# Performance work log

Hardware: AMD Instinct MI355X
Metric: run time of the kernel (lower is better)

The kernel has to match this reference:

```python
import jax, jax.numpy as jnp
import numpy as np

B, P, N, E = 4, 4, 4096, 512
QKV_DIM, HEADS = 512, 8
DH = QKV_DIM // HEADS
EPS = 1e-12  # F.normalize default eps


def setup_inputs() -> dict:
    key = jax.random.key(0)
    ks = jax.random.split(key, 5)
    s = 1.0 / np.sqrt(E)
    return {
        "x": jax.random.normal(ks[0], (B, P, N, E), dtype=jnp.float32),
        "w_qkv": jax.random.normal(ks[1], (3 * QKV_DIM, E), dtype=jnp.float32) * s,
        "b_qkv": jax.random.normal(ks[2], (3 * QKV_DIM,), dtype=jnp.float32) * 0.01,
        "temperature": jnp.ones((HEADS, 1, 1), dtype=jnp.float32),
        "w_out": jax.random.normal(ks[3], (E, QKV_DIM), dtype=jnp.float32) * (1.0 / np.sqrt(QKV_DIM)),
        "b_out": jax.random.normal(ks[4], (E,), dtype=jnp.float32) * 0.01,
    }


def _l2norm(t):
    # F.normalize(t, dim=-1): t / max(||t||_2, eps)
    n = jnp.sqrt(jnp.sum(t * t, axis=-1, keepdims=True))
    return t / jnp.maximum(n, EPS)


def reference(x, w_qkv, b_qkv, temperature, w_out, b_out):
    b, p, n, _ = x.shape
    qkv = x @ w_qkv.T + b_qkv                      # (b,p,n,3*qkv)
    q, k, v = jnp.split(qkv, 3, axis=-1)
    def to_heads(t):
        # (b,p,n,h*dh) -> (b,p,h,dh,n)  (channels-as-tokens)
        t = t.reshape(b, p, n, HEADS, DH)
        return jnp.transpose(t, (0, 1, 3, 4, 2))
    q, k, v = to_heads(q), to_heads(k), to_heads(v)
    q = _l2norm(q)                                  # normalize over tokens n
    k = _l2norm(k)
    # channel-wise (dh x dh) attention per head, temperature-scaled
    attn = jnp.einsum('bphdn,bphen->bphde', q, k) * temperature  # (b,p,h,dh,dh)
    attn = jax.nn.softmax(attn, axis=-1)
    out = jnp.einsum('bphde,bphen->bphdn', attn, v)               # (b,p,h,dh,n)
    # torch rearrange 'b p h n d -> b p d (h n)' on (b,p,h,dh,n) -> (b,p,n,h*dh)
    out = jnp.transpose(out, (0, 1, 4, 2, 3)).reshape(b, p, n, HEADS * DH)
    return out @ w_out.T + b_out
```

## Files before the change

### kernel.cpp

```cpp
#include <hip/hip_runtime.h>
#include <stdint.h>

typedef unsigned short u16;
typedef __bf16 bf16x8 __attribute__((ext_vector_type(8)));
typedef float f32x4 __attribute__((ext_vector_type(4)));

#define AS1 __attribute__((address_space(1)))
#define AS3 __attribute__((address_space(3)))

__device__ __forceinline__ void gload_lds16(u16* lds_wave_base, const u16* g) {
  __builtin_amdgcn_global_load_lds((AS1 void*)g, (AS3 void*)lds_wave_base, 16, 0, 0);
}

__device__ __forceinline__ u16 f2bf(float f) {
  unsigned int u = __float_as_uint(f);
  u += 0x7fffu + ((u >> 16) & 1u);
  return (u16)(u >> 16);
}

__global__ void cast_f32_bf16(const float* __restrict__ in, u16* __restrict__ out, int n8) {
  int i = blockIdx.x * blockDim.x + threadIdx.x;
  if (i >= n8) return;
  const float4* p = (const float4*)in + (size_t)i * 2;
  float4 a = p[0], b = p[1];
  uint2 lo, hi;
  lo.x = (unsigned)f2bf(a.x) | ((unsigned)f2bf(a.y) << 16);
  lo.y = (unsigned)f2bf(a.z) | ((unsigned)f2bf(a.w) << 16);
  hi.x = (unsigned)f2bf(b.x) | ((unsigned)f2bf(b.y) << 16);
  hi.y = (unsigned)f2bf(b.z) | ((unsigned)f2bf(b.w) << 16);
  uint2* o = (uint2*)out + (size_t)i * 2;
  o[0] = lo;
  o[1] = hi;
}

template <int MODE>
__global__ __launch_bounds__(256) void gemm_bt(const u16* __restrict__ gA,
                                               const u16* __restrict__ gB,
                                               const float* __restrict__ bias,
                                               void* __restrict__ gC,
                                               float* __restrict__ ssq) {
  __shared__ __align__(16) u16 smem[128 * 136];
  u16* As = smem;
  u16* Bs = smem + 4096;
  const int t = threadIdx.x;
  const int w = t >> 6, l = t & 63;
  const int lrow = l & 15, quad = l >> 4;
  const int wm = (w >> 1) * 64, wn = (w & 1) * 64;
  int m0, n0, zz = 0;
  if (MODE == 0) {
    const int b = blockIdx.x;
    const int ch = (b >> 3) & 7;
    const int T = ((b >> 6) << 3) | (b & 7);
    m0 = T * 128;
    n0 = ch * 128;
  } else if (MODE == 1) {
    const int b = blockIdx.x;
    const int j = (b >> 3) & 3;
    const int T = ((b >> 5) << 3) | (b & 7);
    m0 = j * 128;
    n0 = T * 128;
  } else {
    const int b = blockIdx.x;
    const int local = b & 127;
    zz = b >> 7;
    const int j = (local >> 3) & 3;
    const int T = ((local >> 5) << 3) | (local & 7);
    m0 = j * 128;
    n0 = T * 128;
  }
  const u16* pA = gA;
  const u16* pB = gB;
  if (MODE == 2) {
    pA += (size_t)zz * (512 * 512);
    pB += (size_t)zz * (4096 * 512);
  }
  const int srow = w * 32 + (l >> 2);
  const int scol = (l & 3) * 8;
  const u16* ga0 = pA + (size_t)(m0 + srow) * 512 + scol;
  const u16* ga1 = pA + (size_t)(m0 + srow + 16) * 512 + scol;
  const u16* gb0 = pB + (size_t)(n0 + srow) * 512 + scol;
  const u16* gb1 = pB + (size_t)(n0 + srow + 16) * 512 + scol;
  u16* lA0 = &As[w * 1024];
  u16* lA1 = &As[w * 1024 + 512];
  u16* lB0 = &Bs[w * 1024];
  u16* lB1 = &Bs[w * 1024 + 512];

  f32x4 acc[4][4];
#pragma unroll
  for (int mi = 0; mi < 4; ++mi)
#pragma unroll
    for (int ni = 0; ni < 4; ++ni) acc[mi][ni] = (f32x4){0.f, 0.f, 0.f, 0.f};

#pragma unroll 1
  for (int k0 = 0; k0 < 512; k0 += 32) {
    gload_lds16(lA0, ga0 + k0);
    gload_lds16(lA1, ga1 + k0);
    gload_lds16(lB0, gb0 + k0);
    gload_lds16(lB1, gb1 + k0);
    __syncthreads();
    bf16x8 af[4], bfr[4];
#pragma unroll
    for (int mi = 0; mi < 4; ++mi)
      af[mi] = *(const bf16x8*)&As[(wm + mi * 16 + lrow) * 32 + quad * 8];
#pragma unroll
    for (int ni = 0; ni < 4; ++ni)
      bfr[ni] = *(const bf16x8*)&Bs[(wn + ni * 16 + lrow) * 32 + quad * 8];
#pragma unroll
    for (int mi = 0; mi < 4; ++mi)
#pragma unroll
      for (int ni = 0; ni < 4; ++ni)
        acc[mi][ni] = __builtin_amdgcn_mfma_f32_16x16x32_bf16(af[mi], bfr[ni], acc[mi][ni], 0, 0, 0);
    __syncthreads();
  }

  if (MODE == 2) {
    float* fs = (float*)smem;
#pragma unroll
    for (int half = 0; half < 2; ++half) {
      if (half) __syncthreads();
#pragma unroll
      for (int mi = 0; mi < 4; ++mi) {
        const int mrow_l = wm + mi * 16 + quad * 4;
        const float4 bb = *(const float4*)&bias[m0 + mrow_l];
#pragma unroll
        for (int ni = 0; ni < 4; ++ni) {
          const int ncol_l = wn + ni * 16 + lrow;
          if ((ncol_l >> 6) != half) continue;
          f32x4 v = acc[mi][ni];
          float4 o;
          o.x = v[0] + bb.x;
          o.y = v[1] + bb.y;
          o.z = v[2] + bb.z;
          o.w = v[3] + bb.w;
          *(float4*)&fs[(ncol_l & 63) * 136 + mrow_l] = o;
        }
      }
      __syncthreads();
#pragma unroll
      for (int j2 = 0; j2 < 4; ++j2) {
        const int g = j2 * 256 + t;
        const int r = g >> 4;
        const int c = (g & 15) * 8;
        float4 v0 = *(const float4*)&fs[r * 136 + c];
        float4 v1 = *(const float4*)&fs[r * 136 + c + 4];
        float* yp = (float*)gC + (((size_t)zz * 4096 + n0 + half * 64 + r) * 512 + m0 + c);
        *(float4*)yp = v0;
        *(float4*)(yp + 4) = v1;
      }
    }
  } else {
    float ss[4] = {0.f, 0.f, 0.f, 0.f};
#pragma unroll
    for (int mi = 0; mi < 4; ++mi) {
      const int mrow_l = wm + mi * 16 + quad * 4;
#pragma unroll
      for (int ni = 0; ni < 4; ++ni) {
        const int ncol_l = wn + ni * 16 + lrow;
        f32x4 v = acc[mi][ni];
        float f0, f1, f2, f3;
        if (MODE == 0) {
          const float bb = bias[n0 + ncol_l];
          f0 = v[0] + bb;
          f1 = v[1] + bb;
          f2 = v[2] + bb;
          f3 = v[3] + bb;
          ss[ni] += f0 * f0 + f1 * f1 + f2 * f2 + f3 * f3;
        } else {
          const float4 bb = *(const float4*)&bias[1024 + m0 + mrow_l];
          f0 = v[0] + bb.x;
          f1 = v[1] + bb.y;
          f2 = v[2] + bb.z;
          f3 = v[3] + bb.w;
        }
        uint2 pk;
        pk.x = (unsigned)f2bf(f0) | ((unsigned)f2bf(f1) << 16);
        pk.y = (unsigned)f2bf(f2) | ((unsigned)f2bf(f3) << 16);
        *(uint2*)&smem[ncol_l * 136 + mrow_l] = pk;
      }
    }
    if (MODE == 0) {
#pragma unroll
      for (int ni = 0; ni < 4; ++ni) {
        float s = ss[ni];
        s += __shfl_xor(s, 16);
        s += __shfl_xor(s, 32);
        if (quad == 0)
          atomicAdd(&ssq[((m0 >> 12) << 10) + n0 + wn + ni * 16 + lrow], s);
      }
    }
    __syncthreads();
    u16* outp = (u16*)gC;
#pragma unroll
    for (int j = 0; j < 8; ++j) {
      const int g = j * 256 + t;
      const int r = g >> 4;
      const int c = (g & 15) * 8;
      uint4 val = *(const uint4*)&smem[r * 136 + c];
      size_t gaddr;
      if (MODE == 0) {
        gaddr = ((size_t)(m0 >> 12) << 22) + ((size_t)(n0 + r) << 12) + (size_t)((m0 & 4095) + c);
      } else {
        const int tokg = n0 + r;
        gaddr = (size_t)(tokg >> 12) * (4096 * 512) + (size_t)(tokg & 4095) * 512 + (size_t)(m0 + c);
      }
      *(uint4*)(outp + gaddr) = val;
    }
  }
}

__global__ __launch_bounds__(256) void qk_partial(const u16* __restrict__ QKt,
                                                  float* __restrict__ part) {
  __shared__ __align__(16) float sred[64 * 64];
  const int b = blockIdx.x;
  const int chunk = b & 7, blk = b >> 3;
  const int bp = blk >> 3, h = blk & 7;
  const int t = threadIdx.x, w = t >> 6, l = t & 63;
  const int lrow = l & 15, quad = l >> 4;
  const u16* base = QKt + ((size_t)bp << 22);
  const u16* qb = base + ((size_t)(h * 64) << 12);
  const u16* kb = base + ((size_t)(512 + h * 64) << 12);
  f32x4 acc[4][4];
#pragma unroll
  for (int mi = 0; mi < 4; ++mi)
#pragma unroll
    for (int ni = 0; ni < 4; ++ni) acc[mi][ni] = (f32x4){0.f, 0.f, 0.f, 0.f};
  const int nbase = chunk * 512 + w * 128;
#pragma unroll 1
  for (int ks = 0; ks < 4; ++ks) {
    const int nn = nbase + ks * 32 + quad * 8;
    bf16x8 af[4], bfr[4];
#pragma unroll
    for (int mi = 0; mi < 4; ++mi)
      af[mi] = *(const bf16x8*)(qb + (((size_t)(mi * 16 + lrow)) << 12) + nn);
#pragma unroll
    for (int ni = 0; ni < 4; ++ni)
      bfr[ni] = *(const bf16x8*)(kb + (((size_t)(ni * 16 + lrow)) << 12) + nn);
#pragma unroll
    for (int mi = 0; mi < 4; ++mi)
#pragma unroll
      for (int ni = 0; ni < 4; ++ni)
        acc[mi][ni] = __builtin_amdgcn_mfma_f32_16x16x32_bf16(af[mi], bfr[ni], acc[mi][ni], 0, 0, 0);
  }
  __syncthreads();
  for (int ww = 0; ww < 4; ++ww) {
    if (w == ww) {
#pragma unroll
      for (int mi = 0; mi < 4; ++mi)
#pragma unroll
        for (int ni = 0; ni < 4; ++ni)
#pragma unroll
          for (int r = 0; r < 4; ++r) {
            const int idx = (mi * 16 + quad * 4 + r) * 64 + ni * 16 + lrow;
            if (ww == 0)
              sred[idx] = acc[mi][ni][r];
            else
              sred[idx] += acc[mi][ni][r];
          }
    }
    __syncthreads();
  }
  float4* dst = (float4*)(part + ((size_t)blk * 8 + chunk) * 4096);
  const float4* src = (const float4*)sred;
  for (int i = t; i < 1024; i += 256) dst[i] = src[i];
}

__global__ __launch_bounds__(512) void softmax_weff(const float* __restrict__ part,
                                                    const u16* __restrict__ wout,
                                                    const float* __restrict__ temperature,
                                                    const float* __restrict__ ssq,
                                                    u16* __restrict__ Weff) {
  __shared__ __align__(16) float sattn[64 * 64];
  __shared__ __align__(16) u16 sattnT[64 * 64];
  __shared__ float rn[128];
  const int blk = blockIdx.x;
  const int bp = blk >> 3, h = blk & 7;
  const int t = threadIdx.x, w = t >> 6, l = t & 63;
  const int lrow = l & 15, quad = l >> 4;

  const float4* pbase = (const float4*)(part + (size_t)blk * 8 * 4096);
  for (int i = t; i < 1024; i += 512) {
    float4 s0 = pbase[i];
#pragma unroll
    for (int p = 1; p < 8; ++p) {
      float4 sp = pbase[p * 1024 + i];
      s0.x += sp.x;
      s0.y += sp.y;
      s0.z += sp.z;
      s0.w += sp.w;
    }
    ((float4*)sattn)[i] = s0;
  }

  if (t < 128) {
    const int ch = (t < 64) ? (h * 64 + t) : (448 + h * 64 + t);
    const float nn = sqrtf(ssq[(bp << 10) + ch]);
    rn[t] = 1.f / fmaxf(nn, 1e-12f);
  }
  __syncthreads();

  if (t < 64) {
    const int d = t;
    const float rq = rn[d];
    const float tmp = temperature[h];
    float mx = -1e30f;
    for (int e = 0; e < 64; ++e) {
      const int idx = (e + d) & 63;
      float v = sattn[d * 64 + idx] * rq * rn[64 + idx] * tmp;
      sattn[d * 64 + idx] = v;
      mx = fmaxf(mx, v);
    }
    float s = 0.f;
    for (int e = 0; e < 64; ++e) {
      const int idx = (e + d) & 63;
      float p = __expf(sattn[d * 64 + idx] - mx);
      s += p;
      sattn[d * 64 + idx] = p;
    }
    const float inv = 1.f / s;
    for (int e = 0; e < 64; ++e) sattnT[e * 64 + d] = f2bf(sattn[d * 64 + e] * inv);
  }
  __syncthreads();

  bf16x8 a0[4], a1[4];
#pragma unroll
  for (int mi = 0; mi < 4; ++mi) {
    a0[mi] = *(const bf16x8*)&sattnT[(mi * 16 + lrow) * 64 + quad * 8];
    a1[mi] = *(const bf16x8*)&sattnT[(mi * 16 + lrow) * 64 + 32 + quad * 8];
  }
  u16* wb = Weff + ((size_t)bp * (512 * 512));
#pragma unroll 1
  for (int nb = 0; nb < 4; ++nb) {
    const int co = (w * 4 + nb) * 16 + lrow;
    const u16* wrow = wout + (size_t)co * 512 + h * 64;
    bf16x8 b0 = *(const bf16x8*)(wrow + quad * 8);
    bf16x8 b1 = *(const bf16x8*)(wrow + 32 + quad * 8);
#pragma unroll
    for (int mi = 0; mi < 4; ++mi) {
      f32x4 c = (f32x4){0.f, 0.f, 0.f, 0.f};
      c = __builtin_amdgcn_mfma_f32_16x16x32_bf16(a0[mi], b0, c, 0, 0, 0);
      c = __builtin_amdgcn_mfma_f32_16x16x32_bf16(a1[mi], b1, c, 0, 0, 0);
      const int e0 = mi * 16 + quad * 4;
      uint2 pk;
      pk.x = (unsigned)f2bf(c[0]) | ((unsigned)f2bf(c[1]) << 16);
      pk.y = (unsigned)f2bf(c[2]) | ((unsigned)f2bf(c[3]) << 16);
      *(uint2*)(wb + (size_t)co * 512 + h * 64 + e0) = pk;
    }
  }
}

extern "C" void kernel_launch(void* const* d_in, const int* in_sizes, int n_in,
                              void* d_out, int out_size, void* d_ws, size_t ws_size,
                              hipStream_t stream) {
  const float* x      = (const float*)d_in[0];
  const float* w_qkv  = (const float*)d_in[1];
  const float* b_qkv  = (const float*)d_in[2];
  const float* temp   = (const float*)d_in[3];
  const float* w_out  = (const float*)d_in[4];
  const float* b_out  = (const float*)d_in[5];
  float* y = (float*)d_out;

  char* ws = (char*)d_ws;
  u16* x_bf    = (u16*)(ws);
  u16* wqkv_bf = (u16*)(ws + 67108864);
  u16* wout_bf = (u16*)(ws + 68681728);
  u16* QKt     = (u16*)(ws + 69206016);
  u16* V_nat   = (u16*)(ws + 203423744);
  u16* Weff    = (u16*)(ws + 270532608);
  float* ssq   = (float*)(ws + 278921216);
  float* part  = (float*)(ws);

  hipMemsetAsync(ssq, 0, 16 * 1024 * sizeof(float), stream);
  cast_f32_bf16<<<16384, 256, 0, stream>>>(x, x_bf, 33554432 / 8);
  cast_f32_bf16<<<384, 256, 0, stream>>>(w_qkv, wqkv_bf, 786432 / 8);
  cast_f32_bf16<<<128, 256, 0, stream>>>(w_out, wout_bf, 262144 / 8);

  gemm_bt<0><<<4096, 256, 0, stream>>>(x_bf, wqkv_bf, b_qkv, QKt, ssq);
  gemm_bt<1><<<2048, 256, 0, stream>>>(wqkv_bf + 1024 * 512, x_bf, b_qkv, V_nat, nullptr);
  qk_partial<<<1024, 256, 0, stream>>>(QKt, part);
  softmax_weff<<<128, 512, 0, stream>>>(part, wout_bf, temp, ssq, Weff);
  gemm_bt<2><<<2048, 256, 0, stream>>>(Weff, V_nat, b_out, y, nullptr);
}
```

Before: 509.7 us.

## Reassociate attention via input Gram matrix and fold projections into a fused weight

The QKV projection over all tokens is replaced by the per-(b,p) Gram matrix S = X^T X (512x512, split-K with a reduction kernel). Q·K^T is then derived as Wq S Wk^T plus bias correction terms, and the token L2 norms come from diag(W S W^T) plus column sums of x. The V projection is folded into a combined weight M = Weff·Wv, so the final pass is a single GEMM of x with M plus a precomputed bias vector. This removes the large Q/K/V intermediates and their GEMMs at the cost of a transposed copy of x, a 4096-deep Gram GEMM, a hi/lo bf16 split of S to limit precision loss, and several extra small kernels.

```diff
diff --git a/kernel.cpp b/kernel.cpp
--- a/kernel.cpp
+++ b/kernel.cpp
@@ -16,6 +16,11 @@
   unsigned int u = __float_as_uint(f);
   u += 0x7fffu + ((u >> 16) & 1u);
   return (u16)(u >> 16);
+}
+__device__ __forceinline__ float bf2f(u16 h) { return __uint_as_float(((unsigned)h) << 16); }
+
+__device__ __forceinline__ int swz(int e, int n) {
+  return e * 136 + (((n >> 3) ^ (e & 15)) << 3) + (n & 7);
 }
 
 __global__ void cast_f32_bf16(const float* __restrict__ in, u16* __restrict__ out, int n8) {
@@ -33,12 +38,91 @@
   o[1] = hi;
 }
 
+__global__ __launch_bounds__(256) void cast_x_dual(const float* __restrict__ x,
+                                                   u16* __restrict__ xbf,
+                                                   u16* __restrict__ xbfT,
+                                                   float* __restrict__ svec) {
+  __shared__ __align__(16) u16 sm[128 * 136];
+  const int b = blockIdx.x;
+  const int bp = b >> 7;
+  const int tt = (b >> 2) & 31;
+  const int et = b & 3;
+  const int t = threadIdx.x;
+  const int n0 = tt * 128, e0 = et * 128;
+  const int rsub = t >> 5;
+  const int c4 = (t & 31) * 4;
+  float cs0 = 0.f, cs1 = 0.f, cs2 = 0.f, cs3 = 0.f;
+  const float* xb = x + ((size_t)bp * 4096 + n0) * 512 + e0;
+  u16* ob = xbf + ((size_t)bp * 4096 + n0) * 512 + e0;
+#pragma unroll
+  for (int j = 0; j < 16; ++j) {
+    const int r = j * 8 + rsub;
+    float4 v = *(const float4*)(xb + (size_t)r * 512 + c4);
+    u16 b0 = f2bf(v.x), b1 = f2bf(v.y), b2 = f2bf(v.z), b3 = f2bf(v.w);
+    uint2 pk;
+    pk.x = (unsigned)b0 | ((unsigned)b1 << 16);
+    pk.y = (unsigned)b2 | ((unsigned)b3 << 16);
+    *(uint2*)(ob + (size_t)r * 512 + c4) = pk;
+    sm[(c4 + 0) * 136 + ((j ^ ((c4 + 0) & 15)) << 3) + rsub] = b0;
+    sm[(c4 + 1) * 136 + ((j ^ ((c4 + 1) & 15)) << 3) + rsub] = b1;
+    sm[(c4 + 2) * 136 + ((j ^ ((c4 + 2) & 15)) << 3) + rsub] = b2;
+    sm[(c4 + 3) * 136 + ((j ^ ((c4 + 3) & 15)) << 3) + rsub] = b3;
+    cs0 += v.x; cs1 += v.y; cs2 += v.z; cs3 += v.w;
+  }
+  cs0 += __shfl_xor(cs0, 32);
+  cs1 += __shfl_xor(cs1, 32);
+  cs2 += __shfl_xor(cs2, 32);
+  cs3 += __shfl_xor(cs3, 32);
+  if ((t & 63) < 32) {
+    float* sp = svec + (size_t)bp * 512 + e0 + c4;
+    atomicAdd(sp + 0, cs0);
+    atomicAdd(sp + 1, cs1);
+    atomicAdd(sp + 2, cs2);
+    atomicAdd(sp + 3, cs3);
+  }
+  __syncthreads();
+  u16* otb = xbfT + ((size_t)bp * 512 + e0) * 4096 + n0;
+#pragma unroll
+  for (int j = 0; j < 8; ++j) {
+    const int re = j * 16 + (t >> 4);
+    const int ct8 = t & 15;
+    uint4 v = *(const uint4*)&sm[re * 136 + ((ct8 ^ (re & 15)) << 3)];
+    *(uint4*)(otb + (size_t)re * 4096 + ct8 * 8) = v;
+  }
+}
+
+__global__ __launch_bounds__(256) void transpose_wv(const float* __restrict__ wv,
+                                                    u16* __restrict__ wvT) {
+  __shared__ __align__(16) u16 sm[128 * 136];
+  const int b = blockIdx.x;
+  const int r0 = (b >> 2) * 128;
+  const int c0 = (b & 3) * 128;
+  const int t = threadIdx.x;
+  const int rsub = t >> 5, c4 = (t & 31) * 4;
+#pragma unroll
+  for (int j = 0; j < 16; ++j) {
+    const int r = j * 8 + rsub;
+    float4 v = *(const float4*)(wv + (size_t)(r0 + r) * 512 + c0 + c4);
+    sm[(c4 + 0) * 136 + ((j ^ ((c4 + 0) & 15)) << 3) + rsub] = f2bf(v.x);
+    sm[(c4 + 1) * 136 + ((j ^ ((c4 + 1) & 15)) << 3) + rsub] = f2bf(v.y);
+    sm[(c4 + 2) * 136 + ((j ^ ((c4 + 2) & 15)) << 3) + rsub] = f2bf(v.z);
+    sm[(c4 + 3) * 136 + ((j ^ ((c4 + 3) & 15)) << 3) + rsub] = f2bf(v.w);
+  }
+  __syncthreads();
+#pragma unroll
+  for (int j = 0; j < 8; ++j) {
+    const int re = j * 16 + (t >> 4);
+    const int ct8 = t & 15;
+    uint4 v = *(const uint4*)&sm[re * 136 + ((ct8 ^ (re & 15)) << 3)];
+    *(uint4*)(wvT + (size_t)(c0 + re) * 512 + r0 + ct8 * 8) = v;
+  }
+}
+
 template <int MODE>
-__global__ __launch_bounds__(256) void gemm_bt(const u16* __restrict__ gA,
-                                               const u16* __restrict__ gB,
-                                               const float* __restrict__ bias,
-                                               void* __restrict__ gC,
-                                               float* __restrict__ ssq) {
+__global__ __launch_bounds__(256) void gemm5(const u16* __restrict__ gA,
+                                             const u16* __restrict__ gB,
+                                             const float* __restrict__ bias,
+                                             void* __restrict__ gC) {
   __shared__ __align__(16) u16 smem[128 * 136];
   u16* As = smem;
   u16* Bs = smem + 4096;
@@ -46,44 +130,61 @@
   const int w = t >> 6, l = t & 63;
   const int lrow = l & 15, quad = l >> 4;
   const int wm = (w >> 1) * 64, wn = (w & 1) * 64;
-  int m0, n0, zz = 0;
+  int m0, n0, bp = 0, kc = 0;
   if (MODE == 0) {
     const int b = blockIdx.x;
-    const int ch = (b >> 3) & 7;
-    const int T = ((b >> 6) << 3) | (b & 7);
-    m0 = T * 128;
-    n0 = ch * 128;
+    bp = b >> 6;
+    kc = b & 3;
+    const int tl = (b >> 2) & 15;
+    m0 = (tl >> 2) * 128;
+    n0 = (tl & 3) * 128;
   } else if (MODE == 1) {
     const int b = blockIdx.x;
-    const int j = (b >> 3) & 3;
-    const int T = ((b >> 5) << 3) | (b & 7);
-    m0 = j * 128;
-    n0 = T * 128;
+    bp = b >> 5;
+    const int tl = b & 31;
+    m0 = (tl >> 2) * 128;
+    n0 = (tl & 3) * 128;
+  } else if (MODE == 2) {
+    const int b = blockIdx.x;
+    bp = b >> 4;
+    const int tl = b & 15;
+    m0 = (tl >> 2) * 128;
+    n0 = (tl & 3) * 128;
   } else {
     const int b = blockIdx.x;
     const int local = b & 127;
-    zz = b >> 7;
+    bp = b >> 7;
     const int j = (local >> 3) & 3;
     const int T = ((local >> 5) << 3) | (local & 7);
     m0 = j * 128;
     n0 = T * 128;
   }
+  constexpr int LDA = (MODE == 0) ? 4096 : 512;
+  constexpr int LDB = (MODE == 0) ? 4096 : 512;
   const u16* pA = gA;
   const u16* pB = gB;
-  if (MODE == 2) {
-    pA += (size_t)zz * (512 * 512);
-    pB += (size_t)zz * (4096 * 512);
+  if (MODE == 0) {
+    pA += (size_t)bp * (512 * 4096);
+    pB = pA;
+  } else if (MODE == 1) {
+    pB += (size_t)bp * (512 * 512);
+  } else if (MODE == 2) {
+    pA += (size_t)bp * (512 * 512);
+  } else {
+    pA += (size_t)bp * (512 * 512);
+    pB += (size_t)bp * (4096 * 512);
   }
   const int srow = w * 32 + (l >> 2);
   const int scol = (l & 3) * 8;
-  const u16* ga0 = pA + (size_t)(m0 + srow) * 512 + scol;
-  const u16* ga1 = pA + (size_t)(m0 + srow + 16) * 512 + scol;
-  const u16* gb0 = pB + (size_t)(n0 + srow) * 512 + scol;
-  const u16* gb1 = pB + (size_t)(n0 + srow + 16) * 512 + scol;
+  const int koff = (MODE == 0) ? kc * 1024 : 0;
+  const u16* ga0 = pA + (size_t)(m0 + srow) * LDA + scol + koff;
+  const u16* ga1 = ga0 + (size_t)16 * LDA;
+  const u16* gb0 = pB + (size_t)(n0 + srow) * LDB + scol + koff;
+  const u16* gb1 = gb0 + (size_t)16 * LDB;
   u16* lA0 = &As[w * 1024];
-  u16* lA1 = &As[w * 1024 + 512];
+  u16* lA1 = lA0 + 512;
   u16* lB0 = &Bs[w * 1024];
-  u16* lB1 = &Bs[w * 1024 + 512];
+  u16* lB1 = lB0 + 512;
 
   f32x4 acc[4][4];
 #pragma unroll
@@ -91,29 +192,40 @@
 #pragma unroll
     for (int ni = 0; ni < 4; ++ni) acc[mi][ni] = (f32x4){0.f, 0.f, 0.f, 0.f};
 
+  constexpr int KLEN = (MODE == 0) ? 1024 : 512;
+  constexpr int NPH = (MODE == 1) ? 2 : 1;
 #pragma unroll 1
-  for (int k0 = 0; k0 < 512; k0 += 32) {
-    gload_lds16(lA0, ga0 + k0);
-    gload_lds16(lA1, ga1 + k0);
-    gload_lds16(lB0, gb0 + k0);
-    gload_lds16(lB1, gb1 + k0);
-    __syncthreads();
-    bf16x8 af[4], bfr[4];
-#pragma unroll
-    for (int mi = 0; mi < 4; ++mi)
-      af[mi] = *(const bf16x8*)&As[(wm + mi * 16 + lrow) * 32 + quad * 8];
-#pragma unroll
-    for (int ni = 0; ni < 4; ++ni)
-      bfr[ni] = *(const bf16x8*)&Bs[(wn + ni * 16 + lrow) * 32 + quad * 8];
-#pragma unroll
-    for (int mi = 0; mi < 4; ++mi)
+  for (int ph = 0; ph < NPH; ++ph) {
+    const size_t boff = (MODE == 1) ? (size_t)ph * 4194304 : 0;
+#pragma unroll 1
+    for (int k0 = 0; k0 < KLEN; k0 += 32) {
+      gload_lds16(lA0, ga0 + k0);
+      gload_lds16(lA1, ga1 + k0);
+      gload_lds16(lB0, gb0 + boff + k0);
+      gload_lds16(lB1, gb1 + boff + k0);
+      __syncthreads();
+      bf16x8 af[4], bfr[4];
+#pragma unroll
+      for (int mi = 0; mi < 4; ++mi)
+        af[mi] = *(const bf16x8*)&As[(wm + mi * 16 + lrow) * 32 + quad * 8];
 #pragma unroll
       for (int ni = 0; ni < 4; ++ni)
-        acc[mi][ni] = __builtin_amdgcn_mfma_f32_16x16x32_bf16(af[mi], bfr[ni], acc[mi][ni], 0, 0, 0);
-    __syncthreads();
-  }
-
-  if (MODE == 2) {
+        bfr[ni] = *(const bf16x8*)&Bs[(wn + ni * 16 + lrow) * 32 + quad * 8];
+#pragma unroll
+      for (int mi = 0; mi < 4; ++mi)
+#pragma unroll
+        for (int ni = 0; ni < 4; ++ni)
+          acc[mi][ni] = __builtin_amdgcn_mfma_f32_16x16x32_bf16(af[mi], bfr[ni], acc[mi][ni], 0, 0, 0);
+      __syncthreads();
+    }
+  }
+
+  if (MODE == 0 || MODE == 3) {
+    float* gCp;
+    if (MODE == 0)
+      gCp = (float*)gC + (size_t)(kc * 16 + bp) * 262144;
+    else
+      gCp = (float*)gC + (size_t)bp * (4096 * 512);
     float* fs = (float*)smem;
 #pragma unroll
     for (int half = 0; half < 2; ++half) {
@@ -121,7 +233,8 @@
 #pragma unroll
       for (int mi = 0; mi < 4; ++mi) {
         const int mrow_l = wm + mi * 16 + quad * 4;
-        const float4 bb = *(const float4*)&bias[m0 + mrow_l];
+        float4 bb = {0.f, 0.f, 0.f, 0.f};
+        if (MODE == 3) bb = *(const float4*)&bias[(size_t)bp * 512 + m0 + mrow_l];
 #pragma unroll
         for (int ni = 0; ni < 4; ++ni) {
           const int ncol_l = wn + ni * 16 + lrow;
@@ -143,13 +256,13 @@
         const int c = (g & 15) * 8;
         float4 v0 = *(const float4*)&fs[r * 136 + c];
         float4 v1 = *(const float4*)&fs[r * 136 + c + 4];
-        float* yp = (float*)gC + (((size_t)zz * 4096 + n0 + half * 64 + r) * 512 + m0 + c);
+        float* yp = gCp + ((size_t)(n0 + half * 64 + r) * 512 + m0 + c);
         *(float4*)yp = v0;
         *(float4*)(yp + 4) = v1;
       }
     }
   } else {
-    float ss[4] = {0.f, 0.f, 0.f, 0.f};
+    u16* gCp = (u16*)gC + ((MODE == 1) ? (size_t)bp * 524288 : (size_t)bp * 262144);
 #pragma unroll
     for (int mi = 0; mi < 4; ++mi) {
       const int mrow_l = wm + mi * 16 + quad * 4;
@@ -157,155 +270,143 @@
       for (int ni = 0; ni < 4; ++ni) {
         const int ncol_l = wn + ni * 16 + lrow;
         f32x4 v = acc[mi][ni];
-        float f0, f1, f2, f3;
-        if (MODE == 0) {
-          const float bb = bias[n0 + ncol_l];
-          f0 = v[0] + bb;
-          f1 = v[1] + bb;
-          f2 = v[2] + bb;
-          f3 = v[3] + bb;
-          ss[ni] += f0 * f0 + f1 * f1 + f2 * f2 + f3 * f3;
-        } else {
-          const float4 bb = *(const float4*)&bias[1024 + m0 + mrow_l];
-          f0 = v[0] + bb.x;
-          f1 = v[1] + bb.y;
-          f2 = v[2] + bb.z;
-          f3 = v[3] + bb.w;
-        }
-        uint2 pk;
-        pk.x = (unsigned)f2bf(f0) | ((unsigned)f2bf(f1) << 16);
-        pk.y = (unsigned)f2bf(f2) | ((unsigned)f2bf(f3) << 16);
-        *(uint2*)&smem[ncol_l * 136 + mrow_l] = pk;
+        smem[(mrow_l + 0) * 136 + ncol_l] = f2bf(v[0]);
+        smem[(mrow_l + 1) * 136 + ncol_l] = f2bf(v[1]);
+        smem[(mrow_l + 2) * 136 + ncol_l] = f2bf(v[2]);
+        smem[(mrow_l + 3) * 136 + ncol_l] = f2bf(v[3]);
       }
     }
-    if (MODE == 0) {
-#pragma unroll
-      for (int ni = 0; ni < 4; ++ni) {
-        float s = ss[ni];
-        s += __shfl_xor(s, 16);
-        s += __shfl_xor(s, 32);
-        if (quad == 0)
-          atomicAdd(&ssq[((m0 >> 12) << 10) + n0 + wn + ni * 16 + lrow], s);
-      }
-    }
     __syncthreads();
-    u16* outp = (u16*)gC;
 #pragma unroll
     for (int j = 0; j < 8; ++j) {
       const int g = j * 256 + t;
       const int r = g >> 4;
       const int c = (g & 15) * 8;
       uint4 val = *(const uint4*)&smem[r * 136 + c];
-      size_t gaddr;
-      if (MODE == 0) {
-        gaddr = ((size_t)(m0 >> 12) << 22) + ((size_t)(n0 + r) << 12) + (size_t)((m0 & 4095) + c);
-      } else {
-        const int tokg = n0 + r;
-        gaddr = (size_t)(tokg >> 12) * (4096 * 512) + (size_t)(tokg & 4095) * 512 + (size_t)(m0 + c);
-      }
-      *(uint4*)(outp + gaddr) = val;
-    }
-  }
-}
-
-__global__ __launch_bounds__(256) void qk_partial(const u16* __restrict__ QKt,
-                                                  float* __restrict__ part) {
-  __shared__ __align__(16) float sred[64 * 64];
-  const int b = blockIdx.x;
-  const int chunk = b & 7, blk = b >> 3;
-  const int bp = blk >> 3, h = blk & 7;
-  const int t = threadIdx.x, w = t >> 6, l = t & 63;
-  const int lrow = l & 15, quad = l >> 4;
-  const u16* base = QKt + ((size_t)bp << 22);
-  const u16* qb = base + ((size_t)(h * 64) << 12);
-  const u16* kb = base + ((size_t)(512 + h * 64) << 12);
-  f32x4 acc[4][4];
-#pragma unroll
-  for (int mi = 0; mi < 4; ++mi)
-#pragma unroll
-    for (int ni = 0; ni < 4; ++ni) acc[mi][ni] = (f32x4){0.f, 0.f, 0.f, 0.f};
-  const int nbase = chunk * 512 + w * 128;
-#pragma unroll 1
-  for (int ks = 0; ks < 4; ++ks) {
-    const int nn = nbase + ks * 32 + quad * 8;
-    bf16x8 af[4], bfr[4];
-#pragma unroll
-    for (int mi = 0; mi < 4; ++mi)
-      af[mi] = *(const bf16x8*)(qb + (((size_t)(mi * 16 + lrow)) << 12) + nn);
-#pragma unroll
-    for (int ni = 0; ni < 4; ++ni)
-      bfr[ni] = *(const bf16x8*)(kb + (((size_t)(ni * 16 + lrow)) << 12) + nn);
-#pragma unroll
-    for (int mi = 0; mi < 4; ++mi)
-#pragma unroll
-      for (int ni = 0; ni < 4; ++ni)
-        acc[mi][ni] = __builtin_amdgcn_mfma_f32_16x16x32_bf16(af[mi], bfr[ni], acc[mi][ni], 0, 0, 0);
-  }
-  __syncthreads();
-  for (int ww = 0; ww < 4; ++ww) {
-    if (w == ww) {
-#pragma unroll
-      for (int mi = 0; mi < 4; ++mi)
-#pragma unroll
-        for (int ni = 0; ni < 4; ++ni)
-#pragma unroll
-          for (int r = 0; r < 4; ++r) {
-            const int idx = (mi * 16 + quad * 4 + r) * 64 + ni * 16 + lrow;
-            if (ww == 0)
-              sred[idx] = acc[mi][ni][r];
-            else
-              sred[idx] += acc[mi][ni][r];
-          }
-    }
-    __syncthreads();
-  }
-  float4* dst = (float4*)(part + ((size_t)blk * 8 + chunk) * 4096);
-  const float4* src = (const float4*)sred;
-  for (int i = t; i < 1024; i += 256) dst[i] = src[i];
-}
-
-__global__ __launch_bounds__(512) void softmax_weff(const float* __restrict__ part,
-                                                    const u16* __restrict__ wout,
-                                                    const float* __restrict__ temperature,
-                                                    const float* __restrict__ ssq,
-                                                    u16* __restrict__ Weff) {
+      *(uint4*)(gCp + (size_t)(m0 + r) * 512 + n0 + c) = val;
+    }
+  }
+}
+
+__global__ __launch_bounds__(256) void s4red(const float* __restrict__ Spart,
+                                             u16* __restrict__ Shi) {
+  const size_t i = ((size_t)blockIdx.x * 256 + threadIdx.x) * 4;
+  if (i >= 4194304) return;
+  float4 a = *(const float4*)(Spart + i);
+  float4 b = *(const float4*)(Spart + 4194304 + i);
+  float4 c = *(const float4*)(Spart + 2 * 4194304 + i);
+  float4 d = *(const float4*)(Spart + 3 * 4194304 + i);
+  float s0 = a.x + b.x + c.x + d.x;
+  float s1 = a.y + b.y + c.y + d.y;
+  float s2 = a.z + b.z + c.z + d.z;
+  float s3 = a.w + b.w + c.w + d.w;
+  u16 h0 = f2bf(s0), h1 = f2bf(s1), h2 = f2bf(s2), h3 = f2bf(s3);
+  uint2 hp;
+  hp.x = (unsigned)h0 | ((unsigned)h1 << 16);
+  hp.y = (unsigned)h2 | ((unsigned)h3 << 16);
+  *(uint2*)(Shi + i) = hp;
+  uint2 lp;
+  lp.x = (unsigned)f2bf(s0 - bf2f(h0)) | ((unsigned)f2bf(s1 - bf2f(h1)) << 16);
+  lp.y = (unsigned)f2bf(s2 - bf2f(h2)) | ((unsigned)f2bf(s3 - bf2f(h3)) << 16);
+  *(uint2*)(Shi + 4194304 + i) = lp;
+}
+
+__device__ __forceinline__ void bf8_expand(uint4 v, float* o) {
+  o[0] = bf2f((u16)(v.x & 0xffff)); o[1] = bf2f((u16)(v.x >> 16));
+  o[2] = bf2f((u16)(v.y & 0xffff)); o[3] = bf2f((u16)(v.y >> 16));
+  o[4] = bf2f((u16)(v.z & 0xffff)); o[5] = bf2f((u16)(v.z >> 16));
+  o[6] = bf2f((u16)(v.w & 0xffff)); o[7] = bf2f((u16)(v.w >> 16));
+}
+
+__global__ __launch_bounds__(512) void softmax_weff2(const u16* __restrict__ P,
+                                                     const u16* __restrict__ wqkv,
+                                                     const float* __restrict__ b_qkv,
+                                                     const float* __restrict__ svec,
+                                                     const float* __restrict__ temperature,
+                                                     const u16* __restrict__ wout,
+                                                     u16* __restrict__ Weff) {
   __shared__ __align__(16) float sattn[64 * 64];
   __shared__ __align__(16) u16 sattnT[64 * 64];
-  __shared__ float rn[128];
+  __shared__ float ub[128], dq[128], rnA[128], bb[128];
   const int blk = blockIdx.x;
   const int bp = blk >> 3, h = blk & 7;
   const int t = threadIdx.x, w = t >> 6, l = t & 63;
   const int lrow = l & 15, quad = l >> 4;
 
-  const float4* pbase = (const float4*)(part + (size_t)blk * 8 * 4096);
-  for (int i = t; i < 1024; i += 512) {
-    float4 s0 = pbase[i];
-#pragma unroll
-    for (int p = 1; p < 8; ++p) {
-      float4 sp = pbase[p * 1024 + i];
-      s0.x += sp.x;
-      s0.y += sp.y;
-      s0.z += sp.z;
-      s0.w += sp.w;
-    }
-    ((float4*)sattn)[i] = s0;
-  }
+  {
+    const int mi = w >> 1;
+    const int nip = (w & 1) * 2;
+    const u16* arow = P + ((size_t)bp * 1024 + h * 64 + mi * 16 + lrow) * 512;
+    const u16* brow0 = wqkv + ((size_t)(512 + h * 64 + nip * 16 + lrow)) * 512;
+    const u16* brow1 = brow0 + 16 * 512;
+    f32x4 c0 = (f32x4){0.f, 0.f, 0.f, 0.f};
+    f32x4 c1 = (f32x4){0.f, 0.f, 0.f, 0.f};
+#pragma unroll 1
+    for (int ks = 0; ks < 16; ++ks) {
+      const int ko = ks * 32 + quad * 8;
+      bf16x8 a = *(const bf16x8*)(arow + ko);
+      bf16x8 b0 = *(const bf16x8*)(brow0 + ko);
+      bf16x8 b1 = *(const bf16x8*)(brow1 + ko);
+      c0 = __builtin_amdgcn_mfma_f32_16x16x32_bf16(a, b0, c0, 0, 0, 0);
+      c1 = __builtin_amdgcn_mfma_f32_16x16x32_bf16(a, b1, c1, 0, 0, 0);
+    }
+    const int drow = mi * 16 + quad * 4;
+#pragma unroll
+    for (int r = 0; r < 4; ++r) {
+      sattn[(drow + r) * 64 + nip * 16 + lrow] = c0[r];
+      sattn[(drow + r) * 64 + (nip + 1) * 16 + lrow] = c1[r];
+    }
+  }
+
+  {
+    const int rr = t >> 2, sub = t & 3;
+    const int c = (rr < 64) ? (h * 64 + rr) : (512 + h * 64 + (rr - 64));
+    const u16* prow = P + ((size_t)bp * 1024 + c) * 512 + sub * 128;
+    const u16* wrow = wqkv + (size_t)c * 512 + sub * 128;
+    const float* sv = svec + (size_t)bp * 512 + sub * 128;
+    float accp = 0.f, accu = 0.f;
+#pragma unroll 1
+    for (int i = 0; i < 128; i += 8) {
+      float pf[8], wf[8];
+      bf8_expand(*(const uint4*)(prow + i), pf);
+      bf8_expand(*(const uint4*)(wrow + i), wf);
+      float4 s0 = *(const float4*)(sv + i);
+      float4 s1 = *(const float4*)(sv + i + 4);
+      accp += pf[0] * wf[0] + pf[1] * wf[1] + pf[2] * wf[2] + pf[3] * wf[3] +
+              pf[4] * wf[4] + pf[5] * wf[5] + pf[6] * wf[6] + pf[7] * wf[7];
+      accu += wf[0] * s0.x + wf[1] * s0.y + wf[2] * s0.z + wf[3] * s0.w +
+              wf[4] * s1.x + wf[5] * s1.y + wf[6] * s1.z + wf[7] * s1.w;
+    }
+    accp += __shfl_xor(accp, 1);
+    accp += __shfl_xor(accp, 2);
+    accu += __shfl_xor(accu, 1);
+    accu += __shfl_xor(accu, 2);
+    if (sub == 0) {
+      dq[rr] = accp;
+      ub[rr] = accu;
+    }
+  }
+  __syncthreads();
 
   if (t < 128) {
-    const int ch = (t < 64) ? (h * 64 + t) : (448 + h * 64 + t);
-    const float nn = sqrtf(ssq[(bp << 10) + ch]);
-    rn[t] = 1.f / fmaxf(nn, 1e-12f);
+    const int c = (t < 64) ? (h * 64 + t) : (512 + h * 64 + (t - 64));
+    const float bc = b_qkv[c];
+    const float ss = dq[t] + 2.f * bc * ub[t] + 4096.f * bc * bc;
+    rnA[t] = 1.f / fmaxf(sqrtf(ss), 1e-12f);
+    bb[t] = bc;
   }
   __syncthreads();
 
   if (t < 64) {
     const int d = t;
-    const float rq = rn[d];
+    const float rq = rnA[d], uqv = ub[d], bq = bb[d];
     const float tmp = temperature[h];
     float mx = -1e30f;
     for (int e = 0; e < 64; ++e) {
       const int idx = (e + d) & 63;
-      float v = sattn[d * 64 + idx] * rq * rn[64 + idx] * tmp;
+      const float bk = bb[64 + idx];
+      float g = sattn[d * 64 + idx] + bq * ub[64 + idx] + bk * uqv + 4096.f * bq * bk;
+      float v = g * rq * rnA[64 + idx] * tmp;
       sattn[d * 64 + idx] = v;
       mx = fmaxf(mx, v);
     }
@@ -317,7 +418,10 @@
       sattn[d * 64 + idx] = p;
     }
     const float inv = 1.f / s;
-    for (int e = 0; e < 64; ++e) sattnT[e * 64 + d] = f2bf(sattn[d * 64 + e] * inv);
+    for (int e = 0; e < 64; ++e) {
+      const int idx = (e + d) & 63;
+      sattnT[idx * 64 + d] = f2bf(sattn[d * 64 + idx] * inv);
+    }
   }
   __syncthreads();
 
@@ -348,35 +452,60 @@
   }
 }
 
+__global__ __launch_bounds__(512) void yb_kernel(const u16* __restrict__ Weff,
+                                                 const float* __restrict__ b_qkv,
+                                                 const float* __restrict__ b_out,
+                                                 float* __restrict__ yb) {
+  const int bp = blockIdx.x, co = threadIdx.x;
+  const u16* wr = Weff + ((size_t)bp * 512 + co) * 512;
+  float s = b_out[co];
+#pragma unroll 1
+  for (int i = 0; i < 512; i += 8) {
+    float wf[8];
+    bf8_expand(*(const uint4*)(wr + i), wf);
+    const float4 b0 = *(const float4*)(b_qkv + 1024 + i);
+    const float4 b1 = *(const float4*)(b_qkv + 1024 + i + 4);
+    s += wf[0] * b0.x + wf[1] * b0.y + wf[2] * b0.z + wf[3] * b0.w +
+         wf[4] * b1.x + wf[5] * b1.y + wf[6] * b1.z + wf[7] * b1.w;
+  }
+  yb[(size_t)bp * 512 + co] = s;
+}
+
 extern "C" void kernel_launch(void* const* d_in, const int* in_sizes, int n_in,
                               void* d_out, int out_size, void* d_ws, size_t ws_size,
                               hipStream_t stream) {
-  const float* x      = (const float*)d_in[0];
-  const float* w_qkv  = (const float*)d_in[1];
-  const float* b_qkv  = (const float*)d_in[2];
-  const float* temp   = (const float*)d_in[3];
-  const float* w_out  = (const float*)d_in[4];
-  const float* b_out  = (const float*)d_in[5];
+  const float* x = (const float*)d_in[0];
+  const float* w_qkv = (const float*)d_in[1];
+  const float* b_qkv = (const float*)d_in[2];
+  const float* temp = (const float*)d_in[3];
+  const float* w_out = (const float*)d_in[4];
+  const float* b_out = (const float*)d_in[5];
   float* y = (float*)d_out;
 
   char* ws = (char*)d_ws;
-  u16* x_bf    = (u16*)(ws);
-  u16* wqkv_bf = (u16*)(ws + 67108864);
-  u16* wout_bf = (u16*)(ws + 68681728);
-  u16* QKt     = (u16*)(ws + 69206016);
-  u16* V_nat   = (u16*)(ws + 203423744);
-  u16* Weff    = (u16*)(ws + 270532608);
-  float* ssq   = (float*)(ws + 278921216);
-  float* part  = (float*)(ws);
-
-  hipMemsetAsync(ssq, 0, 16 * 1024 * sizeof(float), stream);
-  cast_f32_bf16<<<16384, 256, 0, stream>>>(x, x_bf, 33554432 / 8);
+  u16* x_bf = (u16*)(ws);
+  u16* x_bfT = (u16*)(ws + 67108864);
+  u16* wqkv_bf = (u16*)(ws + 134217728);
+  u16* wout_bf = (u16*)(ws + 135790592);
+  u16* wvT_bf = (u16*)(ws + 136314880);
+  u16* S_hi = (u16*)(ws + 136839168);
+  u16* P_bf = (u16*)(ws + 153616384);
+  u16* Weff = (u16*)(ws + 170393600);
+  u16* M_bf = (u16*)(ws + 178782208);
+  float* svec = (float*)(ws + 187170816);
+  float* yb = (float*)(ws + 187203584);
+  float* Spart = (float*)(ws + 187236352);
+
+  hipMemsetAsync(svec, 0, 32768, stream);
+  cast_x_dual<<<2048, 256, 0, stream>>>(x, x_bf, x_bfT, svec);
   cast_f32_bf16<<<384, 256, 0, stream>>>(w_qkv, wqkv_bf, 786432 / 8);
   cast_f32_bf16<<<128, 256, 0, stream>>>(w_out, wout_bf, 262144 / 8);
-
-  gemm_bt<0><<<4096, 256, 0, stream>>>(x_bf, wqkv_bf, b_qkv, QKt, ssq);
-  gemm_bt<1><<<2048, 256, 0, stream>>>(wqkv_bf + 1024 * 512, x_bf, b_qkv, V_nat, nullptr);
-  qk_partial<<<1024, 256, 0, stream>>>(QKt, part);
-  softmax_weff<<<128, 512, 0, stream>>>(part, wout_bf, temp, ssq, Weff);
-  gemm_bt<2><<<2048, 256, 0, stream>>>(Weff, V_nat, b_out, y, nullptr);
-}
+  transpose_wv<<<16, 256, 0, stream>>>(w_qkv + 1024 * 512, wvT_bf);
+  gemm5<0><<<1024, 256, 0, stream>>>(x_bfT, x_bfT, nullptr, Spart);
+  s4red<<<4096, 256, 0, stream>>>(Spart, S_hi);
+  gemm5<1><<<512, 256, 0, stream>>>(wqkv_bf, S_hi, nullptr, P_bf);
+  softmax_weff2<<<128, 512, 0, stream>>>(P_bf, wqkv_bf, b_qkv, svec, temp, wout_bf, Weff);
+  yb_kernel<<<16, 512, 0, stream>>>(Weff, b_qkv, b_out, yb);
+  gemm5<2><<<256, 256, 0, stream>>>(Weff, wvT_bf, nullptr, M_bf);
+  gemm5<3><<<2048, 256, 0, stream>>>(M_bf, x_bf, yb, y);
+}
```

Result: slower. 539.5 us (+5.9%).
